# Kernel optimization log

Measured on AMD Instinct MI355X. Metric: run time of the kernel, lower is better.

## Reference

```python
import jax, jax.numpy as jnp
import numpy as np

NUM_HEADS = 8
EPS = 1e-12  # torch F.normalize default eps


def _l2_normalize(t, axis):
    n = jnp.sqrt(jnp.sum(t * t, axis=axis, keepdims=True))
    return t / jnp.maximum(n, EPS)


def setup_inputs() -> dict:
    key = jax.random.key(0)
    k1, k2, k3 = jax.random.split(key, 3)
    B, N, D = 32, 3136, 384
    x = jax.random.normal(k1, (B, N, D), dtype=jnp.float32)
    qkv_w = jax.random.normal(k2, (3 * D, D), dtype=jnp.float32) * (1.0 / np.sqrt(D))
    temperature = jnp.ones((NUM_HEADS, 1, 1), dtype=jnp.float32)
    proj_w = jax.random.normal(k3, (D, D), dtype=jnp.float32) * (1.0 / np.sqrt(D))
    proj_b = jnp.zeros((D,), dtype=jnp.float32)
    return {"x": x, "qkv_w": qkv_w, "temperature": temperature,
            "proj_w": proj_w, "proj_b": proj_b}


def reference(x, qkv_w, temperature, proj_w, proj_b):
    B, N, D = x.shape
    H = NUM_HEADS
    C = D // H
    # qkv projection (no bias), split last dim as (3, H, C) -> (3, B, H, C, N)
    qkv = jnp.einsum('bnd,ed->bne', x, qkv_w)
    qkv = qkv.reshape(B, N, 3, H, C).transpose(2, 0, 3, 4, 1)
    q, k, v = qkv[0], qkv[1], qkv[2]            # each (B, H, C, N)
    q = _l2_normalize(q, axis=-1)               # normalize over tokens N
    k = _l2_normalize(k, axis=-1)
    # cross-covariance attention: (B, H, C, C), scaled by per-head temperature
    attn = jnp.einsum('bhcn,bhdn->bhcd', q, k) * temperature
    attn = jax.nn.softmax(attn, axis=-1)
    out = jnp.einsum('bhcd,bhdn->bhcn', attn, v)  # (B, H, C, N)
    out = out.transpose(0, 3, 1, 2).reshape(B, N, D)
    return jnp.einsum('bnd,ed->bne', out, proj_w) + proj_b
```

## Files before the change

### kernel.cpp

```cpp
#include <hip/hip_runtime.h>


typedef __bf16 bf16x8 __attribute__((ext_vector_type(8)));
typedef float floatx4 __attribute__((ext_vector_type(4)));
typedef unsigned short u16;

#define B_ 32
#define N_ 3136
#define D_ 384
#define H_ 8
#define C_ 48
#define BN_ 100352

__device__ __forceinline__ u16 f2b(float f) {
  unsigned u = __builtin_bit_cast(unsigned, f);
  u += 0x7FFFu + ((u >> 16) & 1u);
  return (u16)(u >> 16);
}
__device__ __forceinline__ void gload16(const u16* g, u16* l) {
  __builtin_amdgcn_global_load_lds(
      (const __attribute__((address_space(1))) void*)g,
      (__attribute__((address_space(3))) void*)l, 16, 0, 0);
}

__global__ __launch_bounds__(256) void k_cvt_t(const float* __restrict__ x,
                                               u16* __restrict__ xbf,
                                               u16* __restrict__ xT) {
  int d0 = blockIdx.x * 64, n0 = blockIdx.y * 64, b = blockIdx.z;
  const float* xp = x + ((size_t)b * N_ + n0) * D_ + d0;
  __shared__ u16 L[64][68];
  int t = threadIdx.x;
  int nl = t >> 4, dl = (t & 15) * 4;
#pragma unroll
  for (int p = 0; p < 4; p++) {
    int n = nl + p * 16;
    float4 v = *(const float4*)(xp + (size_t)n * D_ + dl);
    ushort4 o;
    o.x = f2b(v.x); o.y = f2b(v.y); o.z = f2b(v.z); o.w = f2b(v.w);
    *(ushort4*)(xbf + ((size_t)(b * N_ + n0 + n)) * D_ + d0 + dl) = o;
    *(ushort4*)(&L[n][dl]) = o;
  }
  __syncthreads();
  int dl2 = t >> 4, nl2 = (t & 15) * 4;
#pragma unroll
  for (int p = 0; p < 4; p++) {
    int d = dl2 + p * 16;
    ushort4 o;
    o.x = L[nl2 + 0][d]; o.y = L[nl2 + 1][d];
    o.z = L[nl2 + 2][d]; o.w = L[nl2 + 3][d];
    *(ushort4*)(xT + (size_t)(d0 + d) * BN_ + b * N_ + n0 + nl2) = o;
  }
}

__global__ __launch_bounds__(256) void k_prep(const float* __restrict__ qkv_w,
                                              const float* __restrict__ proj_w,
                                              u16* __restrict__ wbf,
                                              u16* __restrict__ pwbf,
                                              u16* __restrict__ wvT) {
  int blk = blockIdx.x, t = threadIdx.x;
  if (blk < 432) {
    int i = blk * 256 + t;
    float4 v = ((const float4*)qkv_w)[i];
    ushort4 o;
    o.x = f2b(v.x); o.y = f2b(v.y); o.z = f2b(v.z); o.w = f2b(v.w);
    ((ushort4*)wbf)[i] = o;
  } else if (blk < 576) {
    int i = (blk - 432) * 256 + t;
    float4 v = ((const float4*)proj_w)[i];
    ushort4 o;
    o.x = f2b(v.x); o.y = f2b(v.y); o.z = f2b(v.z); o.w = f2b(v.w);
    ((ushort4*)pwbf)[i] = o;
  } else {
    int h = blk - 576;
    for (int idx = t; idx < 384 * 64; idx += 256) {
      int j = idx >> 6, d = idx & 63;
      float v = (d < 48) ? qkv_w[(size_t)(2 * D_ + h * C_ + d) * D_ + j] : 0.f;
      wvT[(size_t)h * 24576 + idx] = f2b(v);
    }
  }
}

__global__ __launch_bounds__(256) void k_gram(const u16* __restrict__ xT,
                                              float* __restrict__ G) {
  int lin = blockIdx.x;
  int w = (lin & 7) * 72 + (lin >> 3);
  int b = w / 18, rem = w % 18;
  int split = rem / 9, tile = rem % 9;
  int m0 = (tile % 3) * 128, n0 = (tile / 3) * 128;
  int kbeg = split * 1600, klen = split ? 1536 : 1600;
  __shared__ u16 As[2][128][32];
  __shared__ u16 Bs[2][128][32];
  int t = threadIdx.x, wid = t >> 6, lane = t & 63;
  int srow = wid * 32 + (lane >> 2), scol = (lane & 3) * 8;
  int wm = (wid & 1) * 64, wn = (wid >> 1) * 64;
  int r = lane & 15, quad = lane >> 4, q8 = quad * 8;
  const u16* base = xT + (size_t)b * N_ + kbeg + scol;
  const u16* gA = base + (size_t)(m0 + srow) * BN_;
  const u16* gB = base + (size_t)(n0 + srow) * BN_;

  floatx4 acc[4][4] = {};
  for (int k0 = 0; k0 < klen; k0 += 64) {
#pragma unroll
    for (int ks = 0; ks < 2; ks++) {
      gload16(gA + k0 + ks * 32,                     &As[ks][wid * 32][0]);
      gload16(gA + k0 + ks * 32 + (size_t)16 * BN_,  &As[ks][wid * 32 + 16][0]);
      gload16(gB + k0 + ks * 32,                     &Bs[ks][wid * 32][0]);
      gload16(gB + k0 + ks * 32 + (size_t)16 * BN_,  &Bs[ks][wid * 32 + 16][0]);
    }
    __syncthreads();
#pragma unroll
    for (int ks = 0; ks < 2; ks++) {
      bf16x8 af[4], bf[4];
#pragma unroll
      for (int i = 0; i < 4; i++) af[i] = *(const bf16x8*)(&As[ks][wm + i * 16 + r][q8]);
#pragma unroll
      for (int j = 0; j < 4; j++) bf[j] = *(const bf16x8*)(&Bs[ks][wn + j * 16 + r][q8]);
#pragma unroll
      for (int i = 0; i < 4; i++)
#pragma unroll
        for (int j = 0; j < 4; j++)
          acc[i][j] = __builtin_amdgcn_mfma_f32_16x16x32_bf16(af[i], bf[j], acc[i][j], 0, 0, 0);
    }
    __syncthreads();
  }
  float* Gp = G + (size_t)split * 4718592 + (size_t)b * 147456;
#pragma unroll
  for (int i = 0; i < 4; i++)
#pragma unroll
    for (int j = 0; j < 4; j++)
#pragma unroll
      for (int v = 0; v < 4; v++) {
        int rr = m0 + wm + i * 16 + quad * 4 + v;
        int cc = n0 + wn + j * 16 + r;
        Gp[(size_t)rr * 384 + cc] = acc[i][j][v];
      }
}

__global__ __launch_bounds__(256) void k_gsum(const float* __restrict__ G,
                                              u16* __restrict__ Gbf) {
  int i = blockIdx.x * 256 + threadIdx.x;
  float4 a = ((const float4*)G)[i];
  float4 b = ((const float4*)(G + 4718592))[i];
  ushort4 o;
  o.x = f2b(a.x + b.x); o.y = f2b(a.y + b.y);
  o.z = f2b(a.z + b.z); o.w = f2b(a.w + b.w);
  ((ushort4*)Gbf)[i] = o;
}

__global__ __launch_bounds__(256) void k_mid1(const u16* __restrict__ wbf,
                                              const u16* __restrict__ Gb,
                                              float* __restrict__ U) {
  int lin = blockIdx.x;
  int w = (lin & 7) * 72 + (lin >> 3);
  int b = w / 18, rem = w % 18;
  int m0 = (rem / 3) * 128, n0 = (rem % 3) * 128;
  __shared__ u16 As[2][128][32];
  __shared__ u16 Bs[2][128][32];
  int t = threadIdx.x, wid = t >> 6, lane = t & 63;
  int srow = wid * 32 + (lane >> 2), scol = (lane & 3) * 8;
  int wm = (wid & 1) * 64, wn = (wid >> 1) * 64;
  int r = lane & 15, quad = lane >> 4, q8 = quad * 8;
  const u16* gA = wbf + (size_t)(m0 + srow) * 384 + scol;
  const u16* gB = Gb + (size_t)b * 147456 + (size_t)(n0 + srow) * 384 + scol;

  floatx4 acc[4][4] = {};
  for (int k0 = 0; k0 < 384; k0 += 64) {
#pragma unroll
    for (int ks = 0; ks < 2; ks++) {
      gload16(gA + k0 + ks * 32,            &As[ks][wid * 32][0]);
      gload16(gA + k0 + ks * 32 + 16 * 384, &As[ks][wid * 32 + 16][0]);
      gload16(gB + k0 + ks * 32,            &Bs[ks][wid * 32][0]);
      gload16(gB + k0 + ks * 32 + 16 * 384, &Bs[ks][wid * 32 + 16][0]);
    }
    __syncthreads();
#pragma unroll
    for (int ks = 0; ks < 2; ks++) {
      bf16x8 af[4], bf[4];
#pragma unroll
      for (int i = 0; i < 4; i++) af[i] = *(const bf16x8*)(&As[ks][wm + i * 16 + r][q8]);
#pragma unroll
      for (int j = 0; j < 4; j++) bf[j] = *(const bf16x8*)(&Bs[ks][wn + j * 16 + r][q8]);
#pragma unroll
      for (int i = 0; i < 4; i++)
#pragma unroll
        for (int j = 0; j < 4; j++)
          acc[i][j] = __builtin_amdgcn_mfma_f32_16x16x32_bf16(af[i], bf[j], acc[i][j], 0, 0, 0);
    }
    __syncthreads();
  }
  float* Ub = U + (size_t)b * 294912;
#pragma unroll
  for (int i = 0; i < 4; i++)
#pragma unroll
    for (int j = 0; j < 4; j++)
#pragma unroll
      for (int v = 0; v < 4; v++) {
        int rr = m0 + wm + i * 16 + quad * 4 + v;
        int cc = n0 + wn + j * 16 + r;
        Ub[(size_t)rr * 384 + cc] = acc[i][j][v];
      }
}

__global__ __launch_bounds__(256) void k_mid2(const float* __restrict__ U,
                                              const u16* __restrict__ wbf,
                                              const u16* __restrict__ wvT,
                                              const float* __restrict__ temp,
                                              u16* __restrict__ MT) {
  int bh = blockIdx.x, b = bh >> 3, h = bh & 7;
  __shared__ __align__(16) u16 sUq[48][32], sUk[48][32], sWq[48][32], sWk[48][32];
  __shared__ __align__(16) u16 sA[48][72];
  __shared__ float sSsq[96];
  __shared__ float sInv[96];
  int t = threadIdx.x, wid = t >> 6, lane = t & 63;
  int r = lane & 15, quad = lane >> 4, q8 = quad * 8;
  const float* Uq = U + (size_t)b * 294912 + (size_t)(h * C_) * 384;
  const float* Uk = U + (size_t)b * 294912 + (size_t)(D_ + h * C_) * 384;
  const u16* Wq = wbf + (size_t)(h * C_) * 384;
  const u16* Wk = wbf + (size_t)(D_ + h * C_) * 384;

  floatx4 accS[3] = {};
  floatx4 accD[6] = {};
  for (int k0 = 0; k0 < 384; k0 += 32) {
    for (int idx = t; idx < 768; idx += 256) {
      int tile = idx / 192, rem = idx - tile * 192;
      int rr = rem >> 2, c8 = (rem & 3) * 8;
      if (tile < 2) {
        const float* src = (tile == 0 ? Uq : Uk) + (size_t)rr * 384 + k0 + c8;
        float4 a = *(const float4*)src;
        float4 bb = *(const float4*)(src + 4);
        ushort4 lo, hi;
        lo.x = f2b(a.x); lo.y = f2b(a.y); lo.z = f2b(a.z); lo.w = f2b(a.w);
        hi.x = f2b(bb.x); hi.y = f2b(bb.y); hi.z = f2b(bb.z); hi.w = f2b(bb.w);
        u16* dst = (tile == 0 ? &sUq[rr][c8] : &sUk[rr][c8]);
        *(ushort4*)dst = lo;
        *(ushort4*)(dst + 4) = hi;
      } else {
        const u16* src = (tile == 2 ? Wq : Wk) + (size_t)rr * 384 + k0 + c8;
        u16* dst = (tile == 2 ? &sWq[rr][c8] : &sWk[rr][c8]);
        *(int4*)dst = *(const int4*)src;
      }
    }
    __syncthreads();
    if (wid < 3) {
      bf16x8 uq = *(const bf16x8*)(&sUq[wid * 16 + r][q8]);
#pragma unroll
      for (int j = 0; j < 3; j++) {
        bf16x8 wk = *(const bf16x8*)(&sWk[j * 16 + r][q8]);
        accS[j] = __builtin_amdgcn_mfma_f32_16x16x32_bf16(uq, wk, accS[j], 0, 0, 0);
      }
    } else {
#pragma unroll
      for (int i = 0; i < 3; i++) {
        bf16x8 uq = *(const bf16x8*)(&sUq[i * 16 + r][q8]);
        bf16x8 wq = *(const bf16x8*)(&sWq[i * 16 + r][q8]);
        bf16x8 uk = *(const bf16x8*)(&sUk[i * 16 + r][q8]);
        bf16x8 wk = *(const bf16x8*)(&sWk[i * 16 + r][q8]);
        accD[i]     = __builtin_amdgcn_mfma_f32_16x16x32_bf16(uq, wq, accD[i], 0, 0, 0);
        accD[3 + i] = __builtin_amdgcn_mfma_f32_16x16x32_bf16(uk, wk, accD[3 + i], 0, 0, 0);
      }
    }
    __syncthreads();
  }
  if (wid == 3) {
#pragma unroll
    for (int i = 0; i < 3; i++)
#pragma unroll
      for (int v = 0; v < 4; v++)
        if (r == quad * 4 + v) {
          sSsq[i * 16 + r] = accD[i][v];
          sSsq[48 + i * 16 + r] = accD[3 + i][v];
        }
  }
  __syncthreads();
  if (t < 96) sInv[t] = 1.f / fmaxf(sqrtf(sSsq[t]), 1e-12f);
  __syncthreads();
  for (int idx = t; idx < 48 * 16; idx += 256) sA[idx >> 4][48 + (idx & 15)] = 0;
  float T = temp[h];
  if (wid < 3) {
    float L[3][4];
    int c_base = wid * 16 + quad * 4;
#pragma unroll
    for (int j = 0; j < 3; j++)
#pragma unroll
      for (int v = 0; v < 4; v++)
        L[j][v] = accS[j][v] * sInv[c_base + v] * sInv[48 + j * 16 + r] * T;
    float mx[4], sum[4];
#pragma unroll
    for (int v = 0; v < 4; v++) mx[v] = fmaxf(fmaxf(L[0][v], L[1][v]), L[2][v]);
#pragma unroll
    for (int m = 1; m <= 8; m <<= 1)
#pragma unroll
      for (int v = 0; v < 4; v++) mx[v] = fmaxf(mx[v], __shfl_xor(mx[v], m));
#pragma unroll
    for (int v = 0; v < 4; v++) sum[v] = 0.f;
#pragma unroll
    for (int j = 0; j < 3; j++)
#pragma unroll
      for (int v = 0; v < 4; v++) { L[j][v] = __expf(L[j][v] - mx[v]); sum[v] += L[j][v]; }
#pragma unroll
    for (int m = 1; m <= 8; m <<= 1)
#pragma unroll
      for (int v = 0; v < 4; v++) sum[v] += __shfl_xor(sum[v], m);
#pragma unroll
    for (int j = 0; j < 3; j++)
#pragma unroll
      for (int v = 0; v < 4; v++)
        sA[c_base + v][j * 16 + r] = f2b(L[j][v] / sum[v]);
  }
  __syncthreads();
  const u16* WvTh = wvT + (size_t)h * 24576;
  floatx4 accM[3][6] = {};
#pragma unroll
  for (int ks = 0; ks < 2; ks++) {
    bf16x8 af[3];
#pragma unroll
    for (int i = 0; i < 3; i++) af[i] = *(const bf16x8*)(&sA[i * 16 + r][ks * 32 + q8]);
#pragma unroll
    for (int jj = 0; jj < 6; jj++) {
      int j = wid * 96 + jj * 16 + r;
      bf16x8 bb = *(const bf16x8*)(WvTh + (size_t)j * 64 + ks * 32 + q8);
#pragma unroll
      for (int i = 0; i < 3; i++)
        accM[i][jj] = __builtin_amdgcn_mfma_f32_16x16x32_bf16(af[i], bb, accM[i][jj], 0, 0, 0);
    }
  }
  u16* MTb = MT + (size_t)b * 147456;
#pragma unroll
  for (int i = 0; i < 3; i++)
#pragma unroll
    for (int jj = 0; jj < 6; jj++)
#pragma unroll
      for (int v = 0; v < 4; v++) {
        int c = i * 16 + quad * 4 + v;
        int j = wid * 96 + jj * 16 + r;
        MTb[(size_t)j * 384 + h * C_ + c] = f2b(accM[i][jj][v]);
      }
}

__global__ __launch_bounds__(256) void k_mid3(const u16* __restrict__ pwbf,
                                              const u16* __restrict__ MT,
                                              u16* __restrict__ R) {
  int m0 = (blockIdx.x % 3) * 128, n0 = (blockIdx.x / 3) * 128, b = blockIdx.y;
  __shared__ u16 As[2][128][32];
  __shared__ u16 Bs[2][128][32];
  int t = threadIdx.x, wid = t >> 6, lane = t & 63;
  int srow = wid * 32 + (lane >> 2), scol = (lane & 3) * 8;
  int wm = (wid & 1) * 64, wn = (wid >> 1) * 64;
  int r = lane & 15, quad = lane >> 4, q8 = quad * 8;
  const u16* gA = pwbf + (size_t)(m0 + srow) * 384 + scol;
  const u16* gB = MT + (size_t)b * 147456 + (size_t)(n0 + srow) * 384 + scol;

  floatx4 acc[4][4] = {};
  for (int k0 = 0; k0 < 384; k0 += 64) {
#pragma unroll
    for (int ks = 0; ks < 2; ks++) {
      gload16(gA + k0 + ks * 32,            &As[ks][wid * 32][0]);
      gload16(gA + k0 + ks * 32 + 16 * 384, &As[ks][wid * 32 + 16][0]);
      gload16(gB + k0 + ks * 32,            &Bs[ks][wid * 32][0]);
      gload16(gB + k0 + ks * 32 + 16 * 384, &Bs[ks][wid * 32 + 16][0]);
    }
    __syncthreads();
#pragma unroll
    for (int ks = 0; ks < 2; ks++) {
      bf16x8 af[4], bf[4];
#pragma unroll
      for (int i = 0; i < 4; i++) af[i] = *(const bf16x8*)(&As[ks][wm + i * 16 + r][q8]);
#pragma unroll
      for (int j = 0; j < 4; j++) bf[j] = *(const bf16x8*)(&Bs[ks][wn + j * 16 + r][q8]);
#pragma unroll
      for (int i = 0; i < 4; i++)
#pragma unroll
        for (int j = 0; j < 4; j++)
          acc[i][j] = __builtin_amdgcn_mfma_f32_16x16x32_bf16(af[i], bf[j], acc[i][j], 0, 0, 0);
    }
    __syncthreads();
  }
  u16* Rb = R + (size_t)b * 147456;
#pragma unroll
  for (int i = 0; i < 4; i++)
#pragma unroll
    for (int j = 0; j < 4; j++)
#pragma unroll
      for (int v = 0; v < 4; v++) {
        int rr = m0 + wm + i * 16 + quad * 4 + v;
        int cc = n0 + wn + j * 16 + r;
        Rb[(size_t)rr * 384 + cc] = f2b(acc[i][j][v]);
      }
}

__global__ __launch_bounds__(256) void k_final(const u16* __restrict__ xbf,
                                               const u16* __restrict__ R,
                                               const float* __restrict__ bias,
                                               float* __restrict__ Y) {
  int lin = blockIdx.y * 3 + blockIdx.x;
  int w = (lin & 7) * 588 + (lin >> 3);
  int ft = w % 3, gt = w / 3;
  int b = gt / 49, n0 = (gt % 49) * 64;
  size_t g0 = (size_t)b * N_ + n0;
  int f0 = ft * 128;
  __shared__ u16 As[2][64][32];
  __shared__ u16 Bs[2][128][32];
  int t = threadIdx.x, wid = t >> 6, lane = t & 63;
  int srow = t >> 2, scol = (t & 3) * 8;
  int wm = (wid & 1) * 32, wn = (wid >> 1) * 64;
  int r = lane & 15, quad = lane >> 4, q8 = quad * 8;
  const u16* gA = xbf + (g0 + srow) * 384 + scol;
  const u16* gB1 = R + (size_t)b * 147456 + (size_t)(f0 + srow) * 384 + scol;
  const u16* gB2 = gB1 + (size_t)64 * 384;

  floatx4 acc[2][4] = {};
  for (int k0 = 0; k0 < 384; k0 += 64) {
#pragma unroll
    for (int ks = 0; ks < 2; ks++) {
      gload16(gA + k0 + ks * 32,  &As[ks][wid * 16][0]);
      gload16(gB1 + k0 + ks * 32, &Bs[ks][wid * 16][0]);
      gload16(gB2 + k0 + ks * 32, &Bs[ks][64 + wid * 16][0]);
    }
    __syncthreads();
#pragma unroll
    for (int ks = 0; ks < 2; ks++) {
      bf16x8 af[2], bf[4];
#pragma unroll
      for (int i = 0; i < 2; i++) af[i] = *(const bf16x8*)(&As[ks][wm + i * 16 + r][q8]);
#pragma unroll
      for (int j = 0; j < 4; j++) bf[j] = *(const bf16x8*)(&Bs[ks][wn + j * 16 + r][q8]);
#pragma unroll
      for (int i = 0; i < 2; i++)
#pragma unroll
        for (int j = 0; j < 4; j++)
          acc[i][j] = __builtin_amdgcn_mfma_f32_16x16x32_bf16(af[i], bf[j], acc[i][j], 0, 0, 0);
    }
    __syncthreads();
  }
#pragma unroll
  for (int i = 0; i < 2; i++)
#pragma unroll
    for (int j = 0; j < 4; j++) {
      int cc = wn + j * 16 + r;
      float bv = bias[f0 + cc];
#pragma unroll
      for (int v = 0; v < 4; v++) {
        int rr = wm + i * 16 + quad * 4 + v;
        Y[(g0 + rr) * 384 + f0 + cc] = acc[i][j][v] + bv;
      }
    }
}

extern "C" void kernel_launch(void* const* d_in, const int* in_sizes, int n_in,
                              void* d_out, int out_size, void* d_ws, size_t ws_size,
                              hipStream_t stream) {
  const float* x      = (const float*)d_in[0];
  const float* qkv_w  = (const float*)d_in[1];
  const float* temp   = (const float*)d_in[2];
  const float* proj_w = (const float*)d_in[3];
  const float* proj_b = (const float*)d_in[4];
  float* out = (float*)d_out;

  char* ws = (char*)d_ws;
  u16*   xbf  = (u16*)(ws);
  u16*   xT   = (u16*)(ws + 77070336);
  u16*   wbf  = (u16*)(ws + 154140672);
  u16*   pwbf = (u16*)(ws + 155025408);
  u16*   wvT  = (u16*)(ws + 155320320);
  float* G    = (float*)(ws + 155713536);
  u16*   Gbf  = (u16*)(ws + 193462272);
  float* U    = (float*)(ws + 202899456);
  u16*   MT   = (u16*)(ws + 240648192);
  u16*   R    = (u16*)(ws + 250085376);

  k_cvt_t<<<dim3(6, 49, 32), 256, 0, stream>>>(x, xbf, xT);
  k_prep<<<584, 256, 0, stream>>>(qkv_w, proj_w, wbf, pwbf, wvT);

  k_gram<<<576, 256, 0, stream>>>(xT, G);
  k_gsum<<<4608, 256, 0, stream>>>(G, Gbf);
  k_mid1<<<576, 256, 0, stream>>>(wbf, Gbf, U);
  k_mid2<<<256, 256, 0, stream>>>(U, wbf, wvT, temp, MT);
  k_mid3<<<dim3(9, 32), 256, 0, stream>>>(pwbf, MT, R);
  k_final<<<dim3(3, 1568), 256, 0, stream>>>(xbf, R, proj_b, out);
}
```

Measured before the change: 494.5 us.

## Exploit Gram symmetry, merge prep kernels, store U in bf16, enlarge final tiles

The cast/transpose kernel and the weight-prep kernel are merged into one launch. The Gram kernel now computes only the six upper-triangular 128x128 tiles, and the sum kernel mirrors them into the full bf16 matrix with scattered transposed stores. The intermediate U is written in bf16 instead of fp32, which halves its traffic and drops the conversion in mid2 at some precision cost. The final GEMM uses 128x128 tiles with a bounds guard on the token edge.

```diff
diff --git a/kernel.cpp b/kernel.cpp
--- a/kernel.cpp
+++ b/kernel.cpp
@@ -23,70 +23,75 @@
       (__attribute__((address_space(3))) void*)l, 16, 0, 0);
 }
 
-__global__ __launch_bounds__(256) void k_cvt_t(const float* __restrict__ x,
+__global__ __launch_bounds__(256) void k_entry(const float* __restrict__ x,
+                                               const float* __restrict__ qkv_w,
+                                               const float* __restrict__ proj_w,
                                                u16* __restrict__ xbf,
-                                               u16* __restrict__ xT) {
-  int d0 = blockIdx.x * 64, n0 = blockIdx.y * 64, b = blockIdx.z;
-  const float* xp = x + ((size_t)b * N_ + n0) * D_ + d0;
-  __shared__ u16 L[64][68];
-  int t = threadIdx.x;
-  int nl = t >> 4, dl = (t & 15) * 4;
-#pragma unroll
-  for (int p = 0; p < 4; p++) {
-    int n = nl + p * 16;
-    float4 v = *(const float4*)(xp + (size_t)n * D_ + dl);
-    ushort4 o;
-    o.x = f2b(v.x); o.y = f2b(v.y); o.z = f2b(v.z); o.w = f2b(v.w);
-    *(ushort4*)(xbf + ((size_t)(b * N_ + n0 + n)) * D_ + d0 + dl) = o;
-    *(ushort4*)(&L[n][dl]) = o;
-  }
-  __syncthreads();
-  int dl2 = t >> 4, nl2 = (t & 15) * 4;
-#pragma unroll
-  for (int p = 0; p < 4; p++) {
-    int d = dl2 + p * 16;
-    ushort4 o;
-    o.x = L[nl2 + 0][d]; o.y = L[nl2 + 1][d];
-    o.z = L[nl2 + 2][d]; o.w = L[nl2 + 3][d];
-    *(ushort4*)(xT + (size_t)(d0 + d) * BN_ + b * N_ + n0 + nl2) = o;
-  }
-}
-
-__global__ __launch_bounds__(256) void k_prep(const float* __restrict__ qkv_w,
-                                              const float* __restrict__ proj_w,
-                                              u16* __restrict__ wbf,
-                                              u16* __restrict__ pwbf,
-                                              u16* __restrict__ wvT) {
-  int blk = blockIdx.x, t = threadIdx.x;
-  if (blk < 432) {
-    int i = blk * 256 + t;
-    float4 v = ((const float4*)qkv_w)[i];
-    ushort4 o;
-    o.x = f2b(v.x); o.y = f2b(v.y); o.z = f2b(v.z); o.w = f2b(v.w);
-    ((ushort4*)wbf)[i] = o;
-  } else if (blk < 576) {
-    int i = (blk - 432) * 256 + t;
-    float4 v = ((const float4*)proj_w)[i];
-    ushort4 o;
-    o.x = f2b(v.x); o.y = f2b(v.y); o.z = f2b(v.z); o.w = f2b(v.w);
-    ((ushort4*)pwbf)[i] = o;
+                                               u16* __restrict__ xT,
+                                               u16* __restrict__ wbf,
+                                               u16* __restrict__ pwbf,
+                                               u16* __restrict__ wvT) {
+  int lin = blockIdx.x, t = threadIdx.x;
+  if (lin < 9408) {
+    int b = lin / 294, rem = lin % 294;
+    int n0 = (rem / 6) * 64, d0 = (rem % 6) * 64;
+    const float* xp = x + ((size_t)b * N_ + n0) * D_ + d0;
+    __shared__ u16 L[64][68];
+    int nl = t >> 4, dl = (t & 15) * 4;
+#pragma unroll
+    for (int p = 0; p < 4; p++) {
+      int n = nl + p * 16;
+      float4 v = *(const float4*)(xp + (size_t)n * D_ + dl);
+      ushort4 o;
+      o.x = f2b(v.x); o.y = f2b(v.y); o.z = f2b(v.z); o.w = f2b(v.w);
+      *(ushort4*)(xbf + ((size_t)(b * N_ + n0 + n)) * D_ + d0 + dl) = o;
+      *(ushort4*)(&L[n][dl]) = o;
+    }
+    __syncthreads();
+    int dl2 = t >> 4, nl2 = (t & 15) * 4;
+#pragma unroll
+    for (int p = 0; p < 4; p++) {
+      int d = dl2 + p * 16;
+      ushort4 o;
+      o.x = L[nl2 + 0][d]; o.y = L[nl2 + 1][d];
+      o.z = L[nl2 + 2][d]; o.w = L[nl2 + 3][d];
+      *(ushort4*)(xT + (size_t)(d0 + d) * BN_ + b * N_ + n0 + nl2) = o;
+    }
   } else {
-    int h = blk - 576;
-    for (int idx = t; idx < 384 * 64; idx += 256) {
-      int j = idx >> 6, d = idx & 63;
-      float v = (d < 48) ? qkv_w[(size_t)(2 * D_ + h * C_ + d) * D_ + j] : 0.f;
-      wvT[(size_t)h * 24576 + idx] = f2b(v);
-    }
-  }
-}
+    int blk = lin - 9408;
+    if (blk < 432) {
+      int i = blk * 256 + t;
+      float4 v = ((const float4*)qkv_w)[i];
+      ushort4 o;
+      o.x = f2b(v.x); o.y = f2b(v.y); o.z = f2b(v.z); o.w = f2b(v.w);
+      ((ushort4*)wbf)[i] = o;
+    } else if (blk < 576) {
+      int i = (blk - 432) * 256 + t;
+      float4 v = ((const float4*)proj_w)[i];
+      ushort4 o;
+      o.x = f2b(v.x); o.y = f2b(v.y); o.z = f2b(v.z); o.w = f2b(v.w);
+      ((ushort4*)pwbf)[i] = o;
+    } else {
+      int h = blk - 576;
+      for (int idx = t; idx < 384 * 64; idx += 256) {
+        int j = idx >> 6, d = idx & 63;
+        float v = (d < 48) ? qkv_w[(size_t)(2 * D_ + h * C_ + d) * D_ + j] : 0.f;
+        wvT[(size_t)h * 24576 + idx] = f2b(v);
+      }
+    }
+  }
+}
+
+__constant__ int c_ti[6] = {0, 0, 0, 1, 1, 2};
+__constant__ int c_tj[6] = {0, 1, 2, 1, 2, 2};
 
 __global__ __launch_bounds__(256) void k_gram(const u16* __restrict__ xT,
                                               float* __restrict__ G) {
   int lin = blockIdx.x;
-  int w = (lin & 7) * 72 + (lin >> 3);
-  int b = w / 18, rem = w % 18;
-  int split = rem / 9, tile = rem % 9;
-  int m0 = (tile % 3) * 128, n0 = (tile / 3) * 128;
+  int w = (lin & 7) * 48 + (lin >> 3);
+  int b = w / 12, rem = w % 12;
+  int split = rem / 6, t6 = rem % 6;
+  int m0 = c_ti[t6] * 128, n0 = c_tj[t6] * 128;
   int kbeg = split * 1600, klen = split ? 1536 : 1600;
   __shared__ u16 As[2][128][32];
   __shared__ u16 Bs[2][128][32];
@@ -123,33 +128,51 @@
     }
     __syncthreads();
   }
-  float* Gp = G + (size_t)split * 4718592 + (size_t)b * 147456;
+  float* Gp = G + ((size_t)split * 192 + b * 6 + t6) * 16384;
 #pragma unroll
   for (int i = 0; i < 4; i++)
 #pragma unroll
     for (int j = 0; j < 4; j++)
 #pragma unroll
       for (int v = 0; v < 4; v++) {
-        int rr = m0 + wm + i * 16 + quad * 4 + v;
-        int cc = n0 + wn + j * 16 + r;
-        Gp[(size_t)rr * 384 + cc] = acc[i][j][v];
+        int rr = wm + i * 16 + quad * 4 + v;
+        int cc = wn + j * 16 + r;
+        Gp[(size_t)rr * 128 + cc] = acc[i][j][v];
       }
 }
 
 __global__ __launch_bounds__(256) void k_gsum(const float* __restrict__ G,
                                               u16* __restrict__ Gbf) {
-  int i = blockIdx.x * 256 + threadIdx.x;
-  float4 a = ((const float4*)G)[i];
-  float4 b = ((const float4*)(G + 4718592))[i];
-  ushort4 o;
-  o.x = f2b(a.x + b.x); o.y = f2b(a.y + b.y);
-  o.z = f2b(a.z + b.z); o.w = f2b(a.w + b.w);
-  ((ushort4*)Gbf)[i] = o;
+  int gid = blockIdx.x, t = threadIdx.x;
+  int tb = gid >> 2, part = gid & 3;
+  int b = tb / 6, t6 = tb % 6;
+  int ti = c_ti[t6], tj = c_tj[t6];
+  const float* G0 = G + ((size_t)b * 6 + t6) * 16384;
+  const float* G1 = G0 + (size_t)192 * 16384;
+  u16* Gb = Gbf + (size_t)b * 147456;
+#pragma unroll
+  for (int it = 0; it < 4; it++) {
+    int idx = part * 1024 + it * 256 + t;
+    int i = idx >> 5, j4 = (idx & 31) * 4;
+    float4 a = ((const float4*)G0)[idx];
+    float4 c = ((const float4*)G1)[idx];
+    float s0 = a.x + c.x, s1 = a.y + c.y, s2 = a.z + c.z, s3 = a.w + c.w;
+    ushort4 o;
+    o.x = f2b(s0); o.y = f2b(s1); o.z = f2b(s2); o.w = f2b(s3);
+    *(ushort4*)(Gb + (size_t)(ti * 128 + i) * 384 + tj * 128 + j4) = o;
+    if (ti != tj) {
+      int cbase = ti * 128 + i;
+      Gb[(size_t)(tj * 128 + j4 + 0) * 384 + cbase] = o.x;
+      Gb[(size_t)(tj * 128 + j4 + 1) * 384 + cbase] = o.y;
+      Gb[(size_t)(tj * 128 + j4 + 2) * 384 + cbase] = o.z;
+      Gb[(size_t)(tj * 128 + j4 + 3) * 384 + cbase] = o.w;
+    }
+  }
 }
 
 __global__ __launch_bounds__(256) void k_mid1(const u16* __restrict__ wbf,
                                               const u16* __restrict__ Gb,
-                                              float* __restrict__ U) {
+                                              u16* __restrict__ Ubf) {
   int lin = blockIdx.x;
   int w = (lin & 7) * 72 + (lin >> 3);
   int b = w / 18, rem = w % 18;
@@ -188,7 +211,7 @@
     }
     __syncthreads();
   }
-  float* Ub = U + (size_t)b * 294912;
+  u16* Ub = Ubf + (size_t)b * 294912;
 #pragma unroll
   for (int i = 0; i < 4; i++)
 #pragma unroll
@@ -197,11 +220,11 @@
       for (int v = 0; v < 4; v++) {
         int rr = m0 + wm + i * 16 + quad * 4 + v;
         int cc = n0 + wn + j * 16 + r;
-        Ub[(size_t)rr * 384 + cc] = acc[i][j][v];
-      }
-}
-
-__global__ __launch_bounds__(256) void k_mid2(const float* __restrict__ U,
+        Ub[(size_t)rr * 384 + cc] = f2b(acc[i][j][v]);
+      }
+}
+
+__global__ __launch_bounds__(256) void k_mid2(const u16* __restrict__ Ubf,
                                               const u16* __restrict__ wbf,
                                               const u16* __restrict__ wvT,
                                               const float* __restrict__ temp,
@@ -213,8 +236,8 @@
   __shared__ float sInv[96];
   int t = threadIdx.x, wid = t >> 6, lane = t & 63;
   int r = lane & 15, quad = lane >> 4, q8 = quad * 8;
-  const float* Uq = U + (size_t)b * 294912 + (size_t)(h * C_) * 384;
-  const float* Uk = U + (size_t)b * 294912 + (size_t)(D_ + h * C_) * 384;
+  const u16* Uq = Ubf + (size_t)b * 294912 + (size_t)(h * C_) * 384;
+  const u16* Uk = Ubf + (size_t)b * 294912 + (size_t)(D_ + h * C_) * 384;
   const u16* Wq = wbf + (size_t)(h * C_) * 384;
   const u16* Wk = wbf + (size_t)(D_ + h * C_) * 384;
 
@@ -224,21 +247,11 @@
     for (int idx = t; idx < 768; idx += 256) {
       int tile = idx / 192, rem = idx - tile * 192;
       int rr = rem >> 2, c8 = (rem & 3) * 8;
-      if (tile < 2) {
-        const float* src = (tile == 0 ? Uq : Uk) + (size_t)rr * 384 + k0 + c8;
-        float4 a = *(const float4*)src;
-        float4 bb = *(const float4*)(src + 4);
-        ushort4 lo, hi;
-        lo.x = f2b(a.x); lo.y = f2b(a.y); lo.z = f2b(a.z); lo.w = f2b(a.w);
-        hi.x = f2b(bb.x); hi.y = f2b(bb.y); hi.z = f2b(bb.z); hi.w = f2b(bb.w);
-        u16* dst = (tile == 0 ? &sUq[rr][c8] : &sUk[rr][c8]);
-        *(ushort4*)dst = lo;
-        *(ushort4*)(dst + 4) = hi;
-      } else {
-        const u16* src = (tile == 2 ? Wq : Wk) + (size_t)rr * 384 + k0 + c8;
-        u16* dst = (tile == 2 ? &sWq[rr][c8] : &sWk[rr][c8]);
-        *(int4*)dst = *(const int4*)src;
-      }
+      const u16* src = (tile == 0 ? Uq : tile == 1 ? Uk : tile == 2 ? Wq : Wk)
+                       + (size_t)rr * 384 + k0 + c8;
+      u16* dst = (tile == 0 ? &sUq[rr][c8] : tile == 1 ? &sUk[rr][c8]
+                  : tile == 2 ? &sWq[rr][c8] : &sWk[rr][c8]);
+      *(int4*)dst = *(const int4*)src;
     }
     __syncthreads();
     if (wid < 3) {
@@ -392,40 +405,40 @@
                                                const u16* __restrict__ R,
                                                const float* __restrict__ bias,
                                                float* __restrict__ Y) {
-  int lin = blockIdx.y * 3 + blockIdx.x;
-  int w = (lin & 7) * 588 + (lin >> 3);
-  int ft = w % 3, gt = w / 3;
-  int b = gt / 49, n0 = (gt % 49) * 64;
-  size_t g0 = (size_t)b * N_ + n0;
+  int lin = blockIdx.x;
+  int w = (lin & 7) * 300 + (lin >> 3);
+  int ft = w % 3, rest = w / 3;
+  int b = rest / 25, gt = rest % 25;
+  size_t g0 = (size_t)b * N_ + gt * 128;
   int f0 = ft * 128;
-  __shared__ u16 As[2][64][32];
+  __shared__ u16 As[2][128][32];
   __shared__ u16 Bs[2][128][32];
   int t = threadIdx.x, wid = t >> 6, lane = t & 63;
-  int srow = t >> 2, scol = (t & 3) * 8;
-  int wm = (wid & 1) * 32, wn = (wid >> 1) * 64;
+  int srow = wid * 32 + (lane >> 2), scol = (lane & 3) * 8;
+  int wm = (wid & 1) * 64, wn = (wid >> 1) * 64;
   int r = lane & 15, quad = lane >> 4, q8 = quad * 8;
   const u16* gA = xbf + (g0 + srow) * 384 + scol;
-  const u16* gB1 = R + (size_t)b * 147456 + (size_t)(f0 + srow) * 384 + scol;
-  const u16* gB2 = gB1 + (size_t)64 * 384;
-
-  floatx4 acc[2][4] = {};
+  const u16* gB = R + (size_t)b * 147456 + (size_t)(f0 + srow) * 384 + scol;
+
+  floatx4 acc[4][4] = {};
   for (int k0 = 0; k0 < 384; k0 += 64) {
 #pragma unroll
     for (int ks = 0; ks < 2; ks++) {
-      gload16(gA + k0 + ks * 32,  &As[ks][wid * 16][0]);
-      gload16(gB1 + k0 + ks * 32, &Bs[ks][wid * 16][0]);
-      gload16(gB2 + k0 + ks * 32, &Bs[ks][64 + wid * 16][0]);
-    }
-    __syncthreads();
-#pragma unroll
-    for (int ks = 0; ks < 2; ks++) {
-      bf16x8 af[2], bf[4];
-#pragma unroll
-      for (int i = 0; i < 2; i++) af[i] = *(const bf16x8*)(&As[ks][wm + i * 16 + r][q8]);
+      gload16(gA + k0 + ks * 32,            &As[ks][wid * 32][0]);
+      gload16(gA + k0 + ks * 32 + 16 * 384, &As[ks][wid * 32 + 16][0]);
+      gload16(gB + k0 + ks * 32,            &Bs[ks][wid * 32][0]);
+      gload16(gB + k0 + ks * 32 + 16 * 384, &Bs[ks][wid * 32 + 16][0]);
+    }
+    __syncthreads();
+#pragma unroll
+    for (int ks = 0; ks < 2; ks++) {
+      bf16x8 af[4], bf[4];
+#pragma unroll
+      for (int i = 0; i < 4; i++) af[i] = *(const bf16x8*)(&As[ks][wm + i * 16 + r][q8]);
 #pragma unroll
       for (int j = 0; j < 4; j++) bf[j] = *(const bf16x8*)(&Bs[ks][wn + j * 16 + r][q8]);
 #pragma unroll
-      for (int i = 0; i < 2; i++)
+      for (int i = 0; i < 4; i++)
 #pragma unroll
         for (int j = 0; j < 4; j++)
           acc[i][j] = __builtin_amdgcn_mfma_f32_16x16x32_bf16(af[i], bf[j], acc[i][j], 0, 0, 0);
@@ -433,15 +446,16 @@
     __syncthreads();
   }
 #pragma unroll
-  for (int i = 0; i < 2; i++)
+  for (int i = 0; i < 4; i++)
 #pragma unroll
     for (int j = 0; j < 4; j++) {
-      int cc = wn + j * 16 + r;
-      float bv = bias[f0 + cc];
+      int cc = f0 + wn + j * 16 + r;
+      float bv = bias[cc];
 #pragma unroll
       for (int v = 0; v < 4; v++) {
         int rr = wm + i * 16 + quad * 4 + v;
-        Y[(g0 + rr) * 384 + f0 + cc] = acc[i][j][v] + bv;
+        if (gt * 128 + rr < N_)
+          Y[(g0 + rr) * 384 + cc] = acc[i][j][v] + bv;
       }
     }
 }
@@ -463,18 +477,16 @@
   u16*   pwbf = (u16*)(ws + 155025408);
   u16*   wvT  = (u16*)(ws + 155320320);
   float* G    = (float*)(ws + 155713536);
-  u16*   Gbf  = (u16*)(ws + 193462272);
-  float* U    = (float*)(ws + 202899456);
-  u16*   MT   = (u16*)(ws + 240648192);
-  u16*   R    = (u16*)(ws + 250085376);
-
-  k_cvt_t<<<dim3(6, 49, 32), 256, 0, stream>>>(x, xbf, xT);
-  k_prep<<<584, 256, 0, stream>>>(qkv_w, proj_w, wbf, pwbf, wvT);
-
-  k_gram<<<576, 256, 0, stream>>>(xT, G);
-  k_gsum<<<4608, 256, 0, stream>>>(G, Gbf);
-  k_mid1<<<576, 256, 0, stream>>>(wbf, Gbf, U);
-  k_mid2<<<256, 256, 0, stream>>>(U, wbf, wvT, temp, MT);
+  u16*   Gbf  = (u16*)(ws + 180879360);
+  u16*   Ubf  = (u16*)(ws + 190316544);
+  u16*   MT   = (u16*)(ws + 209190912);
+  u16*   R    = (u16*)(ws + 218628096);
+
+  k_entry<<<9992, 256, 0, stream>>>(x, qkv_w, proj_w, xbf, xT, wbf, pwbf, wvT);
+  k_gram<<<384, 256, 0, stream>>>(xT, G);
+  k_gsum<<<768, 256, 0, stream>>>(G, Gbf);
+  k_mid1<<<576, 256, 0, stream>>>(wbf, Gbf, Ubf);
+  k_mid2<<<256, 256, 0, stream>>>(Ubf, wbf, wvT, temp, MT);
   k_mid3<<<dim3(9, 32), 256, 0, stream>>>(pwbf, MT, R);
-  k_final<<<dim3(3, 1568), 256, 0, stream>>>(xbf, R, proj_b, out);
-}
+  k_final<<<2400, 256, 0, stream>>>(xbf, R, proj_b, out);
+}
```

Result: no change. 486.9 us (-1.5%).
